# Performance work log

Measured on AMD Instinct MI355X. Metric: run time of the kernel, lower is better.

Reference implementation:

```python
import jax, jax.numpy as jnp
import numpy as np

EMB_DIM = 768
HEAD = 12
HEAD_DIM = EMB_DIM // HEAD


def setup_inputs() -> dict:
    key = jax.random.key(0)
    ks = jax.random.split(key, 6)
    B, N, D = 8, 1024, EMB_DIM
    s = 1.0 / np.sqrt(D)
    return {
        "z": jax.random.normal(ks[0], (B, N, D), dtype=jnp.float32),
        "w_q": jax.random.normal(ks[1], (D, D), dtype=jnp.float32) * s,
        "w_k": jax.random.normal(ks[2], (D, D), dtype=jnp.float32) * s,
        "w_v": jax.random.normal(ks[3], (D, D), dtype=jnp.float32) * s,
        "w_o": jax.random.normal(ks[4], (D, D), dtype=jnp.float32) * s,
        "b_o": jax.random.normal(ks[5], (D,), dtype=jnp.float32) * 0.01,
    }


def reference(z, w_q, w_k, w_v, w_o, b_o):
    B, N, D = z.shape
    sqrt_dh = jnp.asarray(HEAD_DIM, z.dtype) ** 0.5
    # project and split heads: [B, H, N, Dh]
    def heads(x, w):
        return (x @ w.T).reshape(B, N, HEAD, HEAD_DIM).transpose(0, 2, 1, 3)
    q = heads(z, w_q)
    k = heads(z, w_k)
    v = heads(z, w_v)
    dots = jnp.einsum("bhqd,bhkd->bhqk", q, k) / sqrt_dh
    attn = jax.nn.softmax(dots, axis=-1)  # dropout p=0 -> identity
    out = jnp.einsum("bhqk,bhkd->bhqd", attn, v)
    out = out.transpose(0, 2, 1, 3).reshape(B, N, D)
    return out @ w_o.T + b_o
```

## Files before the change

kernel.cpp:

```cpp
#include <hip/hip_runtime.h>
#include <hip/hip_bf16.h>
#include <stdint.h>

typedef unsigned short u16;
typedef __attribute__((ext_vector_type(8))) short bf16x8;
typedef __attribute__((ext_vector_type(4))) float f32x4;

__device__ __forceinline__ u16 f2bf(float f) {
    union { float f; unsigned int i; } c; c.f = f;
    unsigned int x = c.i;
    return (u16)((x + 0x7FFFu + ((x >> 16) & 1u)) >> 16);
}
__device__ __forceinline__ u16 f2bf_fast(float f) {
    union { float f; unsigned int i; } c; c.f = f;
    return (u16)((c.i + 0x8000u) >> 16);
}

__device__ __forceinline__ void glds16(const u16* g, u16* l) {
    __builtin_amdgcn_global_load_lds(
        (const __attribute__((address_space(1))) void*)g,
        (__attribute__((address_space(3))) void*)l, 16, 0, 0);
}

__device__ __forceinline__ void bar() { asm volatile("s_barrier" ::: "memory"); }
template <int N> __device__ __forceinline__ void waitv() {
    if constexpr (N == 0)      asm volatile("s_waitcnt vmcnt(0)" ::: "memory");
    else if constexpr (N == 2) asm volatile("s_waitcnt vmcnt(2)" ::: "memory");
    else if constexpr (N == 3) asm volatile("s_waitcnt vmcnt(3)" ::: "memory");
    else if constexpr (N == 4) asm volatile("s_waitcnt vmcnt(4)" ::: "memory");
}

__global__ __launch_bounds__(256) void convert_all(
    const float* __restrict__ z, const float* __restrict__ wq,
    const float* __restrict__ wk, const float* __restrict__ wv,
    const float* __restrict__ wo,
    u16* __restrict__ zb, u16* __restrict__ wqb, u16* __restrict__ wkb,
    u16* __restrict__ wvb, u16* __restrict__ wob)
{
    int g = blockIdx.x * 256 + threadIdx.x;
    const float* s; u16* d;
    if (g < 786432)       { s = z;  d = zb;  }
    else if (g < 860160)  { s = wq; d = wqb; g -= 786432; }
    else if (g < 933888)  { s = wk; d = wkb; g -= 860160; }
    else if (g < 1007616) { s = wv; d = wvb; g -= 933888; }
    else                  { s = wo; d = wob; g -= 1007616; }
    float4 a = *(const float4*)(s + (size_t)g * 8);
    float4 b = *(const float4*)(s + (size_t)g * 8 + 4);
    u16 t[8] = {f2bf(a.x), f2bf(a.y), f2bf(a.z), f2bf(a.w),
                f2bf(b.x), f2bf(b.y), f2bf(b.z), f2bf(b.w)};
    *(uint4*)(d + (size_t)g * 8) = *(const uint4*)t;
}

template <int MI>
__device__ __forceinline__ void gemm_mainloop(
    const u16* __restrict__ A, const u16* __restrict__ B,
    u16* As, u16* Bs, f32x4 (&acc)[MI][4], int m0, int lda, int ldb, int K)
{
    const int t = threadIdx.x;
    const int w = t >> 6, lane = t & 63, quad = lane >> 4, lc = lane & 15;
    const int wm = w >> 1, wn = w & 1;
    const int swz = (lc >> 1) & 3;
    constexpr int NA = MI / 2;
    constexpr int ASZ = 1024 * MI;

    const u16* pa[NA]; int la[NA];
    #pragma unroll
    for (int j = 0; j < NA; j++) {
        const int c = j * 256 + t;
        const int row = c >> 2;
        const int kq = (c & 3) ^ ((row >> 1) & 3);
        pa[j] = &A[(size_t)(m0 + row) * lda + kq * 8];
        la[j] = (j * 256 + w * 64) * 8;
    }
    const u16* pb[2]; int lb[2];
    #pragma unroll
    for (int j = 0; j < 2; j++) {
        const int c = j * 256 + t;
        const int row = c >> 2;
        const int kq = (c & 3) ^ ((row >> 1) & 3);
        pb[j] = &B[(size_t)row * ldb + kq * 8];
        lb[j] = (j * 256 + w * 64) * 8;
    }

    #pragma unroll
    for (int j = 0; j < NA; j++) glds16(pa[j], As + la[j]);
    #pragma unroll
    for (int j = 0; j < 2; j++) glds16(pb[j], Bs + lb[j]);
    __syncthreads();

    int buf = 0;
    for (int k0 = 0; k0 < K; k0 += 32) {
        if (k0 + 32 < K) {
            const int na = (buf ^ 1) * ASZ, nbb = (buf ^ 1) * 4096;
            #pragma unroll
            for (int j = 0; j < NA; j++) glds16(pa[j] + k0 + 32, As + na + la[j]);
            #pragma unroll
            for (int j = 0; j < 2; j++)  glds16(pb[j] + k0 + 32, Bs + nbb + lb[j]);
        }
        bf16x8 af[MI], bfr[4];
        #pragma unroll
        for (int i = 0; i < MI; i++) {
            const int row = 32 * NA * wm + 16 * i + lc;
            af[i] = *(const bf16x8*)&As[buf * ASZ + (row * 4 + (quad ^ swz)) * 8];
        }
        #pragma unroll
        for (int j = 0; j < 4; j++) {
            const int row = 64 * wn + 16 * j + lc;
            bfr[j] = *(const bf16x8*)&Bs[buf * 4096 + (row * 4 + (quad ^ swz)) * 8];
        }
        #pragma unroll
        for (int i = 0; i < MI; i++)
            #pragma unroll
            for (int j = 0; j < 4; j++)
                acc[i][j] = __builtin_amdgcn_mfma_f32_16x16x32_bf16(af[i], bfr[j], acc[i][j], 0, 0, 0);
        __syncthreads();
        buf ^= 1;
    }
}

__global__ __launch_bounds__(256) void qkv_gemm(
    const u16* __restrict__ zb, const u16* __restrict__ wqb,
    const u16* __restrict__ wkb, const u16* __restrict__ wvb,
    u16* __restrict__ qkb, u16* __restrict__ vt)
{
    __shared__ __align__(16) u16 As[8192], Bs[8192];
    const int d = blockIdx.x;
    const int n0 = (d >> 6) * 128, m0 = (d & 63) * 128;
    const u16* Bp;
    if (n0 < 768)       Bp = wqb + (size_t)n0 * 768;
    else if (n0 < 1536) Bp = wkb + (size_t)(n0 - 768) * 768;
    else                Bp = wvb + (size_t)(n0 - 1536) * 768;

    const int t = threadIdx.x;
    const int w = t >> 6, lane = t & 63, quad = lane >> 4, lc = lane & 15;
    const int wm = w >> 1, wn = w & 1;
    const int swz = (lc >> 1) & 3;

    const u16* pa[2]; const u16* pb[2]; int la[2], lb[2];
    #pragma unroll
    for (int j = 0; j < 2; j++) {
        const int c = j * 256 + t;
        const int row = c >> 2;
        const int kq = (c & 3) ^ ((row >> 1) & 3);
        pa[j] = &zb[(size_t)(m0 + row) * 768 + kq * 8];
        pb[j] = &Bp[(size_t)row * 768 + kq * 8];
        la[j] = lb[j] = (j * 256 + w * 64) * 8;
    }

    glds16(pa[0], As + la[0]);  glds16(pa[1], As + la[1]);
    glds16(pb[0], Bs + lb[0]);  glds16(pb[1], Bs + lb[1]);
    glds16(pa[0] + 32, As + 4096 + la[0]);  glds16(pa[1] + 32, As + 4096 + la[1]);
    glds16(pb[0] + 32, Bs + 4096 + lb[0]);  glds16(pb[1] + 32, Bs + 4096 + lb[1]);

    f32x4 acc[4][4] = {};
    int buf = 0;
    for (int bk = 0; bk < 24; bk++) {
        if (bk + 1 < 24) waitv<4>(); else waitv<0>();
        bar();
        bf16x8 af[4], bfr[4];
        #pragma unroll
        for (int i = 0; i < 4; i++) {
            const int row = 64 * wm + 16 * i + lc;
            af[i] = *(const bf16x8*)&As[buf * 4096 + (row * 4 + (quad ^ swz)) * 8];
        }
        #pragma unroll
        for (int j = 0; j < 4; j++) {
            const int row = 64 * wn + 16 * j + lc;
            bfr[j] = *(const bf16x8*)&Bs[buf * 4096 + (row * 4 + (quad ^ swz)) * 8];
        }
        #pragma unroll
        for (int i = 0; i < 4; i++)
            #pragma unroll
            for (int j = 0; j < 4; j++)
                acc[i][j] = __builtin_amdgcn_mfma_f32_16x16x32_bf16(af[i], bfr[j], acc[i][j], 0, 0, 0);
        bar();
        if (bk + 2 < 24) {
            const int k2 = (bk + 2) * 32;
            glds16(pa[0] + k2, As + buf * 4096 + la[0]);
            glds16(pa[1] + k2, As + buf * 4096 + la[1]);
            glds16(pb[0] + k2, Bs + buf * 4096 + lb[0]);
            glds16(pb[1] + k2, Bs + buf * 4096 + lb[1]);
        }
        buf ^= 1;
    }

    if (n0 < 1536) {
        #pragma unroll
        for (int i = 0; i < 4; i++)
            #pragma unroll
            for (int j = 0; j < 4; j++) {
                const int col = n0 + 64 * wn + 16 * j + lc;
                #pragma unroll
                for (int r = 0; r < 4; r++) {
                    const int row = m0 + 64 * wm + 16 * i + quad * 4 + r;
                    qkb[(size_t)row * 1536 + col] = f2bf_fast(acc[i][j][r]);
                }
            }
    } else {
        #pragma unroll
        for (int i = 0; i < 4; i++)
            #pragma unroll
            for (int j = 0; j < 4; j++) {
                const int c = (n0 - 1536) + 64 * wn + 16 * j + lc;
                const int h = c >> 6, dd = c & 63;
                const int tok0 = m0 + 64 * wm + 16 * i + quad * 4;
                const int b = tok0 >> 10, n = tok0 & 1023;
                ushort4 pk = { f2bf_fast(acc[i][j][0]), f2bf_fast(acc[i][j][1]),
                               f2bf_fast(acc[i][j][2]), f2bf_fast(acc[i][j][3]) };
                *(ushort4*)&vt[(((size_t)(b * 12 + h)) * 64 + dd) * 1024 + n] = pk;
            }
    }
}

__global__ __launch_bounds__(256) void oproj_gemm(
    const u16* __restrict__ ob, const u16* __restrict__ wob,
    const float* __restrict__ bo, float* __restrict__ out)
{
    __shared__ __align__(16) u16 As[4096], Bs[8192];
    const int d = blockIdx.x;
    const int n0 = (d >> 7) * 128, m0 = (d & 127) * 64;
    f32x4 acc[2][4] = {};
    gemm_mainloop<2>(ob, wob + (size_t)n0 * 768, As, Bs, acc, m0, 768, 768, 768);

    const int t = threadIdx.x;
    const int w = t >> 6, lane = t & 63, quad = lane >> 4, lc = lane & 15;
    const int wm = w >> 1, wn = w & 1;
    #pragma unroll
    for (int i = 0; i < 2; i++)
        #pragma unroll
        for (int j = 0; j < 4; j++) {
            const int col = n0 + 64 * wn + 16 * j + lc;
            const float bv = bo[col];
            #pragma unroll
            for (int r = 0; r < 4; r++) {
                const int row = m0 + 32 * wm + 16 * i + quad * 4 + r;
                out[(size_t)row * 768 + col] = acc[i][j][r] + bv;
            }
        }
}

__global__ __launch_bounds__(512, 4) void attn_kernel(
    const u16* __restrict__ qkb, const u16* __restrict__ vt,
    u16* __restrict__ obuf)
{
    const int b = blockIdx.x / 12, h = blockIdx.x % 12;
    const int q0 = blockIdx.y * 128;
    const int t = threadIdx.x;
    const int w = t >> 6, lane = t & 63, quad = lane >> 4, lc = lane & 15;

    const u16* Qp  = qkb + (size_t)b * 1024 * 1536 + h * 64;
    const u16* Kp  = Qp + 768;
    const u16* Vtp = vt + ((size_t)(b * 12 + h)) * 64 * 1024;

    __shared__ __align__(16) u16 U[128 * 136];
    __shared__ __align__(16) u16 Vts[64 * 128];

    const u16* kp[2]; u16* kl[2];
    #pragma unroll
    for (int j = 0; j < 2; j++) {
        const int c = j * 512 + t;
        const int row = c >> 3;
        const int kq = (c & 7) ^ ((row >> 1) & 7);
        kp[j] = Kp + (size_t)row * 1536 + kq * 8;
        kl[j] = &U[(j * 512 + w * 64) * 8];
    }
    const u16* vp[2]; u16* vl[2];
    #pragma unroll
    for (int s2 = 0; s2 < 2; s2++) {
        const int s = 2 * w + s2;
        const int c = s * 64 + lane;
        const int dd = c >> 4, kq = (c & 15) ^ (dd & 15);
        vp[s2] = Vtp + (size_t)dd * 1024 + kq * 8;
        vl[s2] = &Vts[s * 512];
    }

    bf16x8 qf[2];
    #pragma unroll
    for (int kk = 0; kk < 2; kk++)
        qf[kk] = *(const bf16x8*)&Qp[(size_t)(q0 + 16 * w + lc) * 1536 + kk * 32 + quad * 8];

    f32x4 oacc[4] = {};
    float lsum[4] = {0.0f, 0.0f, 0.0f, 0.0f};

    const float cs = 0.18033688011112042f;
    const int swk = (lc >> 1) & 7;

    waitv<0>();
    for (int kt = 0; kt < 8; kt++) {
        const int kb = kt * 128;
        bar();
        #pragma unroll
        for (int j = 0; j < 2; j++)
            glds16(kp[j] + (size_t)kb * 1536, kl[j]);
        #pragma unroll
        for (int s2 = 0; s2 < 2; s2++)
            glds16(vp[s2] + kb, vl[s2]);
        waitv<2>();
        bar();

        f32x4 sacc[8] = {};
        #pragma unroll
        for (int j = 0; j < 8; j++) {
            const int nrow = 16 * j + lc;
            bf16x8 kf0 = *(const bf16x8*)&U[(nrow * 8 + (quad ^ swk)) * 8];
            bf16x8 kf1 = *(const bf16x8*)&U[(nrow * 8 + ((4 + quad) ^ swk)) * 8];
            sacc[j] = __builtin_amdgcn_mfma_f32_16x16x32_bf16(qf[0], kf0, sacc[j], 0, 0, 0);
            sacc[j] = __builtin_amdgcn_mfma_f32_16x16x32_bf16(qf[1], kf1, sacc[j], 0, 0, 0);
        }
        waitv<0>();
        bar();

        #pragma unroll
        for (int j = 0; j < 8; j++)
            #pragma unroll
            for (int r = 0; r < 4; r++) {
                float p = __builtin_amdgcn_exp2f(sacc[j][r] * cs);
                lsum[r] += p;
                U[(16 * w + quad * 4 + r) * 136 + 16 * j + lc] = f2bf_fast(p);
            }

        #pragma unroll
        for (int ks = 0; ks < 4; ks++) {
            bf16x8 pa = *(const bf16x8*)&U[(16 * w + lc) * 136 + ks * 32 + quad * 8];
            #pragma unroll
            for (int jd = 0; jd < 4; jd++) {
                bf16x8 vb = *(const bf16x8*)&Vts[(((16 * jd + lc) << 4) + ((ks * 4 + quad) ^ lc)) * 8];
                oacc[jd] = __builtin_amdgcn_mfma_f32_16x16x32_bf16(pa, vb, oacc[jd], 0, 0, 0);
            }
        }
    }

    #pragma unroll
    for (int off = 1; off < 16; off <<= 1)
        #pragma unroll
        for (int r = 0; r < 4; r++)
            lsum[r] += __shfl_xor(lsum[r], off, 64);

    float invl[4];
    #pragma unroll
    for (int r = 0; r < 4; r++) invl[r] = __builtin_amdgcn_rcpf(lsum[r]);
    #pragma unroll
    for (int jd = 0; jd < 4; jd++)
        #pragma unroll
        for (int r = 0; r < 4; r++) {
            const int row = q0 + 16 * w + quad * 4 + r;
            const int col = h * 64 + 16 * jd + lc;
            obuf[((size_t)b * 1024 + row) * 768 + col] = f2bf_fast(oacc[jd][r] * invl[r]);
        }
}

extern "C" void kernel_launch(void* const* d_in, const int* in_sizes, int n_in,
                              void* d_out, int out_size, void* d_ws, size_t ws_size,
                              hipStream_t stream) {
    const float* z  = (const float*)d_in[0];
    const float* wq = (const float*)d_in[1];
    const float* wk = (const float*)d_in[2];
    const float* wv = (const float*)d_in[3];
    const float* wo = (const float*)d_in[4];
    const float* bo = (const float*)d_in[5];

    u16* ws16 = (u16*)d_ws;
    u16* zb   = ws16;
    u16* wqb  = zb  + 6291456;
    u16* wkb  = wqb + 589824;
    u16* wvb  = wkb + 589824;
    u16* wob  = wvb + 589824;
    u16* vt   = wob + 589824;
    u16* qkb  = (u16*)d_out;
    u16* obuf = zb;
    float* out = (float*)d_out;

    convert_all<<<4224, 256, 0, stream>>>(z, wq, wk, wv, wo, zb, wqb, wkb, wvb, wob);
    qkv_gemm<<<1152, 256, 0, stream>>>(zb, wqb, wkb, wvb, qkb, vt);
    attn_kernel<<<dim3(96, 8), 512, 0, stream>>>(qkb, vt, obuf);
    oproj_gemm<<<768, 256, 0, stream>>>(obuf, wob, bo, out);
}
```

Before: 193.4 us.

## Use 2 waves per block in QKV GEMM with 128x64 per-wave tiles

The QKV projection GEMM now runs with 128 threads (2 waves) per block instead of 4. Each wave computes a 128x64 output tile (8x4 MFMA fragments) instead of 64x64. This doubles per-wave reuse of the B fragments and halves LDS fragment reads per MFMA, at the cost of more accumulator registers and fewer waves to hide latency. Each thread issues twice as many async loads, so the vmcnt wait threshold is raised to 8.

```diff
diff --git a/kernel.cpp b/kernel.cpp
--- a/kernel.cpp
+++ b/kernel.cpp
@@ -28,6 +28,7 @@
     else if constexpr (N == 2) asm volatile("s_waitcnt vmcnt(2)" ::: "memory");
     else if constexpr (N == 3) asm volatile("s_waitcnt vmcnt(3)" ::: "memory");
     else if constexpr (N == 4) asm volatile("s_waitcnt vmcnt(4)" ::: "memory");
+    else if constexpr (N == 8) asm volatile("s_waitcnt vmcnt(8)" ::: "memory");
 }
 
 __global__ __launch_bounds__(256) void convert_all(
@@ -118,7 +119,7 @@
     }
 }
 
-__global__ __launch_bounds__(256) void qkv_gemm(
+__global__ __launch_bounds__(128, 2) void qkv_gemm(
     const u16* __restrict__ zb, const u16* __restrict__ wqb,
     const u16* __restrict__ wkb, const u16* __restrict__ wvb,
     u16* __restrict__ qkb, u16* __restrict__ vt)
@@ -133,77 +134,80 @@
 
     const int t = threadIdx.x;
     const int w = t >> 6, lane = t & 63, quad = lane >> 4, lc = lane & 15;
-    const int wm = w >> 1, wn = w & 1;
     const int swz = (lc >> 1) & 3;
 
-    const u16* pa[2]; const u16* pb[2]; int la[2], lb[2];
-    #pragma unroll
-    for (int j = 0; j < 2; j++) {
-        const int c = j * 256 + t;
+    const u16* pa[4]; const u16* pb[4]; int la[4], lb[4];
+    #pragma unroll
+    for (int j = 0; j < 4; j++) {
+        const int c = j * 128 + t;
         const int row = c >> 2;
         const int kq = (c & 3) ^ ((row >> 1) & 3);
         pa[j] = &zb[(size_t)(m0 + row) * 768 + kq * 8];
         pb[j] = &Bp[(size_t)row * 768 + kq * 8];
-        la[j] = lb[j] = (j * 256 + w * 64) * 8;
-    }
-
-    glds16(pa[0], As + la[0]);  glds16(pa[1], As + la[1]);
-    glds16(pb[0], Bs + lb[0]);  glds16(pb[1], Bs + lb[1]);
-    glds16(pa[0] + 32, As + 4096 + la[0]);  glds16(pa[1] + 32, As + 4096 + la[1]);
-    glds16(pb[0] + 32, Bs + 4096 + lb[0]);  glds16(pb[1] + 32, Bs + 4096 + lb[1]);
-
-    f32x4 acc[4][4] = {};
+        la[j] = lb[j] = (j * 128 + w * 64) * 8;
+    }
+
+    #pragma unroll
+    for (int j = 0; j < 4; j++) glds16(pa[j], As + la[j]);
+    #pragma unroll
+    for (int j = 0; j < 4; j++) glds16(pb[j], Bs + lb[j]);
+    #pragma unroll
+    for (int j = 0; j < 4; j++) glds16(pa[j] + 32, As + 4096 + la[j]);
+    #pragma unroll
+    for (int j = 0; j < 4; j++) glds16(pb[j] + 32, Bs + 4096 + lb[j]);
+
+    f32x4 acc[8][4] = {};
     int buf = 0;
     for (int bk = 0; bk < 24; bk++) {
-        if (bk + 1 < 24) waitv<4>(); else waitv<0>();
-        bar();
-        bf16x8 af[4], bfr[4];
-        #pragma unroll
-        for (int i = 0; i < 4; i++) {
-            const int row = 64 * wm + 16 * i + lc;
+        if (bk + 1 < 24) waitv<8>(); else waitv<0>();
+        bar();
+        bf16x8 af[8], bfr[4];
+        #pragma unroll
+        for (int i = 0; i < 8; i++) {
+            const int row = 16 * i + lc;
             af[i] = *(const bf16x8*)&As[buf * 4096 + (row * 4 + (quad ^ swz)) * 8];
         }
         #pragma unroll
         for (int j = 0; j < 4; j++) {
-            const int row = 64 * wn + 16 * j + lc;
+            const int row = 64 * w + 16 * j + lc;
             bfr[j] = *(const bf16x8*)&Bs[buf * 4096 + (row * 4 + (quad ^ swz)) * 8];
         }
         #pragma unroll
-        for (int i = 0; i < 4; i++)
+        for (int i = 0; i < 8; i++)
             #pragma unroll
             for (int j = 0; j < 4; j++)
                 acc[i][j] = __builtin_amdgcn_mfma_f32_16x16x32_bf16(af[i], bfr[j], acc[i][j], 0, 0, 0);
         bar();
         if (bk + 2 < 24) {
             const int k2 = (bk + 2) * 32;
-            glds16(pa[0] + k2, As + buf * 4096 + la[0]);
-            glds16(pa[1] + k2, As + buf * 4096 + la[1]);
-            glds16(pb[0] + k2, Bs + buf * 4096 + lb[0]);
-            glds16(pb[1] + k2, Bs + buf * 4096 + lb[1]);
+            #pragma unroll
+            for (int j = 0; j < 4; j++) glds16(pa[j] + k2, As + buf * 4096 + la[j]);
+            #pragma unroll
+            for (int j = 0; j < 4; j++) glds16(pb[j] + k2, Bs + buf * 4096 + lb[j]);
         }
         buf ^= 1;
     }
 
     if (n0 < 1536) {
         #pragma unroll
-        for (int i = 0; i < 4; i++)
+        for (int i = 0; i < 8; i++)
             #pragma unroll
             for (int j = 0; j < 4; j++) {
-                const int col = n0 + 64 * wn + 16 * j + lc;
+                const int col = n0 + 64 * w + 16 * j + lc;
                 #pragma unroll
                 for (int r = 0; r < 4; r++) {
-                    const int row = m0 + 64 * wm + 16 * i + quad * 4 + r;
+                    const int row = m0 + 16 * i + quad * 4 + r;
                     qkb[(size_t)row * 1536 + col] = f2bf_fast(acc[i][j][r]);
                 }
             }
     } else {
         #pragma unroll
-        for (int i = 0; i < 4; i++)
+        for (int i = 0; i < 8; i++)
             #pragma unroll
             for (int j = 0; j < 4; j++) {
-                const int c = (n0 - 1536) + 64 * wn + 16 * j + lc;
+                const int c = (n0 - 1536) + 64 * w + 16 * j + lc;
                 const int h = c >> 6, dd = c & 63;
-                const int tok0 = m0 + 64 * wm + 16 * i + quad * 4;
+                const int tok0 = m0 + 16 * i + quad * 4;
                 const int b = tok0 >> 10, n = tok0 & 1023;
                 ushort4 pk = { f2bf_fast(acc[i][j][0]), f2bf_fast(acc[i][j][1]),
                                f2bf_fast(acc[i][j][2]), f2bf_fast(acc[i][j][3]) };
@@ -371,7 +375,7 @@
     float* out = (float*)d_out;
 
     convert_all<<<4224, 256, 0, stream>>>(z, wq, wk, wv, wo, zb, wqb, wkb, wvb, wob);
-    qkv_gemm<<<1152, 256, 0, stream>>>(zb, wqb, wkb, wvb, qkb, vt);
+    qkv_gemm<<<1152, 128, 0, stream>>>(zb, wqb, wkb, wvb, qkb, vt);
     attn_kernel<<<dim3(96, 8), 512, 0, stream>>>(qkb, vt, obuf);
     oproj_gemm<<<768, 256, 0, stream>>>(obuf, wob, bo, out);
 }
```

New measurement: 197.5 us. +2.1%, slower.

## Halve attention block threads so each wave handles two 16-row query groups

Applied to the files above, without the earlier changes.

The attention kernel now launches 256 threads per block instead of 512. Each wave processes 32 query rows as two 16-row groups, so every K and V fragment read from LDS feeds two MFMAs, halving LDS fragment traffic per MFMA. Each thread issues twice as many global-to-LDS loads per tile, and register use per thread roughly doubles (two sets of score and output accumulators). Occupancy is lowered to 3 blocks per CU, which risks weaker latency hiding.

```diff
diff --git a/kernel.cpp b/kernel.cpp
--- a/kernel.cpp
+++ b/kernel.cpp
@@ -28,6 +28,7 @@
     else if constexpr (N == 2) asm volatile("s_waitcnt vmcnt(2)" ::: "memory");
     else if constexpr (N == 3) asm volatile("s_waitcnt vmcnt(3)" ::: "memory");
     else if constexpr (N == 4) asm volatile("s_waitcnt vmcnt(4)" ::: "memory");
+    else if constexpr (N == 8) asm volatile("s_waitcnt vmcnt(8)" ::: "memory");
 }
 
 __global__ __launch_bounds__(256) void convert_all(
@@ -239,7 +240,7 @@
         }
 }
 
-__global__ __launch_bounds__(512, 4) void attn_kernel(
+__global__ __launch_bounds__(256, 3) void attn_kernel(
     const u16* __restrict__ qkb, const u16* __restrict__ vt,
     u16* __restrict__ obuf)
 {
@@ -255,32 +256,35 @@
     __shared__ __align__(16) u16 U[128 * 136];
     __shared__ __align__(16) u16 Vts[64 * 128];
 
-    const u16* kp[2]; u16* kl[2];
-    #pragma unroll
-    for (int j = 0; j < 2; j++) {
-        const int c = j * 512 + t;
+    const u16* kp[4]; u16* kl[4];
+    #pragma unroll
+    for (int j = 0; j < 4; j++) {
+        const int c = j * 256 + t;
         const int row = c >> 3;
         const int kq = (c & 7) ^ ((row >> 1) & 7);
         kp[j] = Kp + (size_t)row * 1536 + kq * 8;
-        kl[j] = &U[(j * 512 + w * 64) * 8];
-    }
-    const u16* vp[2]; u16* vl[2];
-    #pragma unroll
-    for (int s2 = 0; s2 < 2; s2++) {
-        const int s = 2 * w + s2;
+        kl[j] = &U[(j * 256 + w * 64) * 8];
+    }
+    const u16* vp[4]; u16* vl[4];
+    #pragma unroll
+    for (int s2 = 0; s2 < 4; s2++) {
+        const int s = 4 * w + s2;
         const int c = s * 64 + lane;
         const int dd = c >> 4, kq = (c & 15) ^ (dd & 15);
         vp[s2] = Vtp + (size_t)dd * 1024 + kq * 8;
         vl[s2] = &Vts[s * 512];
     }
 
-    bf16x8 qf[2];
-    #pragma unroll
-    for (int kk = 0; kk < 2; kk++)
-        qf[kk] = *(const bf16x8*)&Qp[(size_t)(q0 + 16 * w + lc) * 1536 + kk * 32 + quad * 8];
-
-    f32x4 oacc[4] = {};
-    float lsum[4] = {0.0f, 0.0f, 0.0f, 0.0f};
+    bf16x8 qf[2][2];
+    #pragma unroll
+    for (int rg = 0; rg < 2; rg++)
+        #pragma unroll
+        for (int kk = 0; kk < 2; kk++)
+            qf[rg][kk] = *(const bf16x8*)&Qp[(size_t)(q0 + 32 * w + 16 * rg + lc) * 1536
+                                             + kk * 32 + quad * 8];
+
+    f32x4 oacc[2][4] = {};
+    float lsum[2][4] = {};
 
     const float cs = 0.18033688011112042f;
     const int swk = (lc >> 1) & 7;
@@ -290,42 +294,52 @@
         const int kb = kt * 128;
         bar();
         #pragma unroll
-        for (int j = 0; j < 2; j++)
+        for (int j = 0; j < 4; j++)
             glds16(kp[j] + (size_t)kb * 1536, kl[j]);
         #pragma unroll
-        for (int s2 = 0; s2 < 2; s2++)
+        for (int s2 = 0; s2 < 4; s2++)
             glds16(vp[s2] + kb, vl[s2]);
-        waitv<2>();
-        bar();
-
-        f32x4 sacc[8] = {};
+        waitv<4>();
+        bar();
+
+        f32x4 sacc[2][8] = {};
         #pragma unroll
         for (int j = 0; j < 8; j++) {
             const int nrow = 16 * j + lc;
             bf16x8 kf0 = *(const bf16x8*)&U[(nrow * 8 + (quad ^ swk)) * 8];
             bf16x8 kf1 = *(const bf16x8*)&U[(nrow * 8 + ((4 + quad) ^ swk)) * 8];
-            sacc[j] = __builtin_amdgcn_mfma_f32_16x16x32_bf16(qf[0], kf0, sacc[j], 0, 0, 0);
-            sacc[j] = __builtin_amdgcn_mfma_f32_16x16x32_bf16(qf[1], kf1, sacc[j], 0, 0, 0);
+            #pragma unroll
+            for (int rg = 0; rg < 2; rg++) {
+                sacc[rg][j] = __builtin_amdgcn_mfma_f32_16x16x32_bf16(qf[rg][0], kf0, sacc[rg][j], 0, 0, 0);
+                sacc[rg][j] = __builtin_amdgcn_mfma_f32_16x16x32_bf16(qf[rg][1], kf1, sacc[rg][j], 0, 0, 0);
+            }
         }
         waitv<0>();
         bar();
 
         #pragma unroll
-        for (int j = 0; j < 8; j++)
-            #pragma unroll
-            for (int r = 0; r < 4; r++) {
-                float p = __builtin_amdgcn_exp2f(sacc[j][r] * cs);
-                lsum[r] += p;
-                U[(16 * w + quad * 4 + r) * 136 + 16 * j + lc] = f2bf_fast(p);
-            }
+        for (int rg = 0; rg < 2; rg++)
+            #pragma unroll
+            for (int j = 0; j < 8; j++)
+                #pragma unroll
+                for (int r = 0; r < 4; r++) {
+                    float p = __builtin_amdgcn_exp2f(sacc[rg][j][r] * cs);
+                    lsum[rg][r] += p;
+                    U[(32 * w + 16 * rg + quad * 4 + r) * 136 + 16 * j + lc] = f2bf_fast(p);
+                }
 
         #pragma unroll
         for (int ks = 0; ks < 4; ks++) {
-            bf16x8 pa = *(const bf16x8*)&U[(16 * w + lc) * 136 + ks * 32 + quad * 8];
+            bf16x8 pa[2];
+            #pragma unroll
+            for (int rg = 0; rg < 2; rg++)
+                pa[rg] = *(const bf16x8*)&U[(32 * w + 16 * rg + lc) * 136 + ks * 32 + quad * 8];
             #pragma unroll
             for (int jd = 0; jd < 4; jd++) {
                 bf16x8 vb = *(const bf16x8*)&Vts[(((16 * jd + lc) << 4) + ((ks * 4 + quad) ^ lc)) * 8];
-                oacc[jd] = __builtin_amdgcn_mfma_f32_16x16x32_bf16(pa, vb, oacc[jd], 0, 0, 0);
+                #pragma unroll
+                for (int rg = 0; rg < 2; rg++)
+                    oacc[rg][jd] = __builtin_amdgcn_mfma_f32_16x16x32_bf16(pa[rg], vb, oacc[rg][jd], 0, 0, 0);
             }
         }
     }
@@ -333,20 +347,26 @@
     #pragma unroll
     for (int off = 1; off < 16; off <<= 1)
         #pragma unroll
-        for (int r = 0; r < 4; r++)
-            lsum[r] += __shfl_xor(lsum[r], off, 64);
-
-    float invl[4];
-    #pragma unroll
-    for (int r = 0; r < 4; r++) invl[r] = __builtin_amdgcn_rcpf(lsum[r]);
-    #pragma unroll
-    for (int jd = 0; jd < 4; jd++)
-        #pragma unroll
-        for (int r = 0; r < 4; r++) {
-            const int row = q0 + 16 * w + quad * 4 + r;
-            const int col = h * 64 + 16 * jd + lc;
-            obuf[((size_t)b * 1024 + row) * 768 + col] = f2bf_fast(oacc[jd][r] * invl[r]);
-        }
+        for (int rg = 0; rg < 2; rg++)
+            #pragma unroll
+            for (int r = 0; r < 4; r++)
+                lsum[rg][r] += __shfl_xor(lsum[rg][r], off, 64);
+
+    float invl[2][4];
+    #pragma unroll
+    for (int rg = 0; rg < 2; rg++)
+        #pragma unroll
+        for (int r = 0; r < 4; r++) invl[rg][r] = __builtin_amdgcn_rcpf(lsum[rg][r]);
+    #pragma unroll
+    for (int rg = 0; rg < 2; rg++)
+        #pragma unroll
+        for (int jd = 0; jd < 4; jd++)
+            #pragma unroll
+            for (int r = 0; r < 4; r++) {
+                const int row = q0 + 32 * w + 16 * rg + quad * 4 + r;
+                const int col = h * 64 + 16 * jd + lc;
+                obuf[((size_t)b * 1024 + row) * 768 + col] = f2bf_fast(oacc[rg][jd][r] * invl[rg][r]);
+            }
 }
 
 extern "C" void kernel_launch(void* const* d_in, const int* in_sizes, int n_in,
@@ -372,6 +392,6 @@
 
     convert_all<<<4224, 256, 0, stream>>>(z, wq, wk, wv, wo, zb, wqb, wkb, wvb, wob);
     qkv_gemm<<<1152, 256, 0, stream>>>(zb, wqb, wkb, wvb, qkb, vt);
-    attn_kernel<<<dim3(96, 8), 512, 0, stream>>>(qkb, vt, obuf);
+    attn_kernel<<<dim3(96, 8), 256, 0, stream>>>(qkb, vt, obuf);
     oproj_gemm<<<768, 256, 0, stream>>>(obuf, wob, bo, out);
 }
```

Result: no change. 193.4 us (-0.0%).
